# Kernel tuning notes

Hardware: AMD Instinct MI355X
Metric: run time of the kernel (lower is better)

The kernel has to match this reference:

```python
import jax, jax.numpy as jnp
import numpy as np

EPS = 1e-06
N_ITERATIONS = 10


def _babylonian_rsqrt(x):
    # Division-free Newton-Raphson rsqrt with power-of-100 range scaling.
    x_safe = jnp.clip(x.astype(jnp.float32), 1e-08, None)
    log_x = jnp.log10(x_safe + 1.0)
    scale_exp = jnp.floor(log_x / 2.0) * 2.0
    scale = jnp.power(10.0, scale_exp)
    x_norm = x_safe / scale
    y = jnp.full_like(x_norm, 0.1)
    half_x = 0.5 * x_norm
    for _ in range(N_ITERATIONS):
        y = y * (1.5 - half_x * (y * y))
    inv_sqrt_scale = jnp.power(10.0, -scale_exp / 2.0)
    return y * inv_sqrt_scale


def setup_inputs() -> dict:
    key = jax.random.key(0)
    k1, _ = jax.random.split(key)
    B, S, H = 4, 4096, 4096
    x = jax.random.normal(k1, (B, S, H), dtype=jnp.float32)
    weight = jnp.ones((H,), dtype=jnp.float32)
    return {"x": x, "weight": weight}


def reference(x, weight):
    input_dtype = x.dtype
    x_fp32 = x.astype(jnp.float32)
    variance = jnp.mean(x_fp32 * x_fp32, axis=-1, keepdims=True)  # [B, S, 1]
    variance = jnp.clip(variance, 1e-08, None)
    inv_rms = _babylonian_rsqrt(variance + EPS)
    result = x_fp32 * inv_rms * weight.astype(jnp.float32)
    return result.astype(input_dtype)
```

## Files before the change

### kernel.cpp

```cpp
#include <hip/hip_runtime.h>


typedef float f32x4 __attribute__((ext_vector_type(4)));

constexpr int H = 4096;
constexpr int THREADS = 256;
constexpr int VECS_PER_THREAD = H / (THREADS * 4);

__global__ __launch_bounds__(THREADS)
void rational_rmsnorm_kernel(const float* __restrict__ x,
                             const float* __restrict__ w,
                             float* __restrict__ out) {
    const long long row = blockIdx.x;
    const f32x4* xr = reinterpret_cast<const f32x4*>(x + row * (long long)H);
    f32x4* outr     = reinterpret_cast<f32x4*>(out + row * (long long)H);
    const f32x4* wv4 = reinterpret_cast<const f32x4*>(w);

    const int t = threadIdx.x;

    f32x4 v[VECS_PER_THREAD];
    float sumsq = 0.0f;
#pragma unroll
    for (int i = 0; i < VECS_PER_THREAD; ++i) {
        v[i] = __builtin_nontemporal_load(&xr[i * THREADS + t]);
        sumsq += v[i].x * v[i].x + v[i].y * v[i].y
               + v[i].z * v[i].z + v[i].w * v[i].w;
    }

#pragma unroll
    for (int off = 32; off > 0; off >>= 1)
        sumsq += __shfl_down(sumsq, off, 64);

    __shared__ float partial[THREADS / 64];
    const int wave = t >> 6;
    if ((t & 63) == 0) partial[wave] = sumsq;
    __syncthreads();

    float total = partial[0] + partial[1] + partial[2] + partial[3];
    float variance = total * (1.0f / (float)H);
    variance = fmaxf(variance, 1e-8f);
    float xs = variance + 1e-6f;
    xs = fmaxf(xs, 1e-8f);
    float log_x = log10f(xs + 1.0f);
    float scale_exp = floorf(log_x / 2.0f) * 2.0f;
    float scale = powf(10.0f, scale_exp);
    float x_norm = xs / scale;
    float y = 0.1f;
    float half_x = 0.5f * x_norm;
#pragma unroll
    for (int i = 0; i < 10; ++i)
        y = y * (1.5f - half_x * (y * y));
    float inv_sqrt_scale = powf(10.0f, -scale_exp / 2.0f);
    const float inv = y * inv_sqrt_scale;

#pragma unroll
    for (int i = 0; i < VECS_PER_THREAD; ++i) {
        f32x4 wv = wv4[i * THREADS + t];
        f32x4 o = v[i] * inv * wv;
        __builtin_nontemporal_store(o, &outr[i * THREADS + t]);
    }
}

extern "C" void kernel_launch(void* const* d_in, const int* in_sizes, int n_in,
                              void* d_out, int out_size, void* d_ws, size_t ws_size,
                              hipStream_t stream) {
    const float* x = (const float*)d_in[0];
    const float* w = (const float*)d_in[1];
    float* out = (float*)d_out;
    const int nrows = in_sizes[0] / H;
    rational_rmsnorm_kernel<<<nrows, THREADS, 0, stream>>>(x, w, out);
}
```

Baseline: 91.94 us.

## Map one row per wavefront and drop block-level reduction barrier

Each wavefront now handles a whole row, so the sum of squares is reduced with a butterfly shuffle and the shared-memory partials and __syncthreads are removed. The weight vector is loaded up front together with x instead of in the store loop. In exchange each lane holds 16 x vectors and 16 weight vectors in registers, which raises register pressure and may cut occupancy. The grid becomes a quarter as many blocks, and it assumes the row count is divisible by four.

```diff
diff --git a/kernel.cpp b/kernel.cpp
--- a/kernel.cpp
+++ b/kernel.cpp
@@ -5,39 +5,41 @@
 
 constexpr int H = 4096;
 constexpr int THREADS = 256;
-constexpr int VECS_PER_THREAD = H / (THREADS * 4);
+constexpr int WAVES_PER_BLOCK = THREADS / 64;
+constexpr int VECS_PER_LANE = H / (64 * 4);
 
 __global__ __launch_bounds__(THREADS)
 void rational_rmsnorm_kernel(const float* __restrict__ x,
                              const float* __restrict__ w,
                              float* __restrict__ out) {
-    const long long row = blockIdx.x;
+    const int wave = threadIdx.x >> 6;
+    const int lane = threadIdx.x & 63;
+    const long long row = (long long)blockIdx.x * WAVES_PER_BLOCK + wave;
+
     const f32x4* xr = reinterpret_cast<const f32x4*>(x + row * (long long)H);
     f32x4* outr     = reinterpret_cast<f32x4*>(out + row * (long long)H);
     const f32x4* wv4 = reinterpret_cast<const f32x4*>(w);
 
-    const int t = threadIdx.x;
+    f32x4 v[VECS_PER_LANE];
+    f32x4 wv[VECS_PER_LANE];
+#pragma unroll
+    for (int i = 0; i < VECS_PER_LANE; ++i)
+        v[i] = __builtin_nontemporal_load(&xr[i * 64 + lane]);
+#pragma unroll
+    for (int i = 0; i < VECS_PER_LANE; ++i)
+        wv[i] = wv4[i * 64 + lane];
 
-    f32x4 v[VECS_PER_THREAD];
     float sumsq = 0.0f;
 #pragma unroll
-    for (int i = 0; i < VECS_PER_THREAD; ++i) {
-        v[i] = __builtin_nontemporal_load(&xr[i * THREADS + t]);
+    for (int i = 0; i < VECS_PER_LANE; ++i)
         sumsq += v[i].x * v[i].x + v[i].y * v[i].y
                + v[i].z * v[i].z + v[i].w * v[i].w;
-    }
 
 #pragma unroll
     for (int off = 32; off > 0; off >>= 1)
-        sumsq += __shfl_down(sumsq, off, 64);
+        sumsq += __shfl_xor(sumsq, off, 64);
 
-    __shared__ float partial[THREADS / 64];
-    const int wave = t >> 6;
-    if ((t & 63) == 0) partial[wave] = sumsq;
-    __syncthreads();
-
-    float total = partial[0] + partial[1] + partial[2] + partial[3];
-    float variance = total * (1.0f / (float)H);
+    float variance = sumsq * (1.0f / (float)H);
     variance = fmaxf(variance, 1e-8f);
     float xs = variance + 1e-6f;
     xs = fmaxf(xs, 1e-8f);
@@ -54,10 +56,9 @@
     const float inv = y * inv_sqrt_scale;
 
 #pragma unroll
-    for (int i = 0; i < VECS_PER_THREAD; ++i) {
-        f32x4 wv = wv4[i * THREADS + t];
-        f32x4 o = v[i] * inv * wv;
-        __builtin_nontemporal_store(o, &outr[i * THREADS + t]);
+    for (int i = 0; i < VECS_PER_LANE; ++i) {
+        f32x4 o = v[i] * inv * wv[i];
+        __builtin_nontemporal_store(o, &outr[i * 64 + lane]);
     }
 }
 
@@ -68,5 +69,5 @@
     const float* w = (const float*)d_in[1];
     float* out = (float*)d_out;
     const int nrows = in_sizes[0] / H;
-    rational_rmsnorm_kernel<<<nrows, THREADS, 0, stream>>>(x, w, out);
+    rational_rmsnorm_kernel<<<nrows / WAVES_PER_BLOCK, THREADS, 0, stream>>>(x, w, out);
 }
```

After: 93.88 us. 2.1% more time.
